# Performance work log

Hardware: AMD Instinct MI355X
Metric: run time of the kernel (lower is better)

The kernel has to match this reference:

```python
import jax, jax.numpy as jnp
import numpy as np

B, L, E, H = 32, 2048, 512, 512


def setup_inputs() -> dict:
    key = jax.random.key(0)
    k1, k2, k3, k4 = jax.random.split(key, 4)
    encodings = jax.random.normal(k1, (B, L, E), dtype=jnp.float32)
    lengths = jax.random.randint(k2, (B,), 1, L + 1, dtype=jnp.int32)
    # Glorot-ish scaled params
    W_h = jax.random.normal(k3, (E, H), dtype=jnp.float32) / np.sqrt(E)
    b_h = jnp.zeros((H,), dtype=jnp.float32)
    W_c = jax.random.normal(k4, (H, E), dtype=jnp.float32) / np.sqrt(H)
    return {"encodings": encodings, "lengths": lengths, "W_h": W_h, "b_h": b_h, "W_c": W_c}


def reference(encodings, lengths, W_h, b_h, W_c):
    # encodings: [B, L, E] padded ragged pack; lengths: [B] valid lengths
    mask = jnp.arange(encodings.shape[1])[None, :] < lengths[:, None]  # [B, L]
    # hidden_layer with tanh nonlinearity (TimeDistributedLinear)
    h = jnp.tanh(jnp.einsum('ble,eh->blh', encodings, W_h) + b_h)  # [B, L, H]
    # context_vector (no bias) -> per-feature attention logits [B, L, E]
    att = jnp.einsum('blh,he->ble', h, W_c)
    # timedistributed_softmax: softmax over time axis per sample, per feature
    att = jnp.where(mask[:, :, None], att, -jnp.inf)
    att = jax.nn.softmax(att, axis=1)  # padded positions get weight 0
    # weighted sum over time -> [B, E], then unsqueeze(1)
    out = jnp.sum(att * encodings, axis=1)[:, None, :]  # [B, 1, E]
    return out
```

## Files before the change

### kernel.cpp

```cpp
#include <hip/hip_runtime.h>
#include <math.h>

#define BB 32
#define LL 2048
#define EE 512
#define HH 512

typedef __bf16 bf16_t;
typedef bf16_t bf16x8 __attribute__((ext_vector_type(8)));
typedef float f32x4 __attribute__((ext_vector_type(4)));
typedef unsigned short u16x8 __attribute__((ext_vector_type(8)));

__device__ __forceinline__ unsigned short f2bf(float f) {
  unsigned int u = __builtin_bit_cast(unsigned int, f);
  unsigned int r = (u + 0x7FFFu + ((u >> 16) & 1u)) >> 16;
  return (unsigned short)r;
}
__device__ __forceinline__ float bf2f(unsigned short s) {
  unsigned int u = ((unsigned int)s) << 16;
  return __builtin_bit_cast(float, u);
}
__device__ __forceinline__ bf16x8 ld_frag(const unsigned short* p) {
  u16x8 raw = *(const u16x8*)p;
  return __builtin_bit_cast(bf16x8, raw);
}
__device__ __forceinline__ float tanh_fast(float x) {
  x = fminf(fmaxf(x, -15.f), 15.f);
  float e2 = __expf(2.f * x);
  return (e2 - 1.f) / (e2 + 1.f);
}

__device__ __forceinline__ void frag_issue(const unsigned short* __restrict__ g,
                                           int k0, bf16x8 f[4]) {
#pragma unroll
  for (int i = 0; i < 4; i++) f[i] = ld_frag(g + (size_t)i * 16 * 512 + k0);
}

#define G1_HALF(F, W, PF, PFB) do {                                             \
    if (PF) frag_issue(baseW, (((W) + 3 + phase) & 15) * 32, PFB);              \
    const int k0_ = (((W) + phase) & 15) * 32;                                  \
    const bf16x8 b0_ = ld_frag(&encA[(l15     ) * 520 + k0_ + quad * 8]);       \
    const bf16x8 b1_ = ld_frag(&encA[(16 + l15) * 520 + k0_ + quad * 8]);       \
    const bf16x8 b2_ = ld_frag(&encA[(32 + l15) * 520 + k0_ + quad * 8]);       \
    const bf16x8 b3_ = ld_frag(&encA[(48 + l15) * 520 + k0_ + quad * 8]);       \
    _Pragma("unroll")                                                           \
    for (int t_ = 0; t_ < 4; t_++) {                                            \
      acc[t_ * 4 + 0] = __builtin_amdgcn_mfma_f32_16x16x32_bf16(F[t_], b0_, acc[t_ * 4 + 0], 0, 0, 0); \
      acc[t_ * 4 + 1] = __builtin_amdgcn_mfma_f32_16x16x32_bf16(F[t_], b1_, acc[t_ * 4 + 1], 0, 0, 0); \
      acc[t_ * 4 + 2] = __builtin_amdgcn_mfma_f32_16x16x32_bf16(F[t_], b2_, acc[t_ * 4 + 2], 0, 0, 0); \
      acc[t_ * 4 + 3] = __builtin_amdgcn_mfma_f32_16x16x32_bf16(F[t_], b3_, acc[t_ * 4 + 3], 0, 0, 0); \
    }                                                                           \
  } while (0)

#define G2_HALF(F, W, PF, PFB) do {                                             \
    if (PF) frag_issue(baseW, (((W) + 3 + phase) & 15) * 32, PFB);              \
    const int k0_ = (((W) + phase) & 15) * 32;                                  \
    const bf16x8 a0_ = ld_frag(&hS[(l15     ) * 520 + k0_ + quad * 8]);         \
    const bf16x8 a1_ = ld_frag(&hS[(16 + l15) * 520 + k0_ + quad * 8]);         \
    const bf16x8 a2_ = ld_frag(&hS[(32 + l15) * 520 + k0_ + quad * 8]);         \
    const bf16x8 a3_ = ld_frag(&hS[(48 + l15) * 520 + k0_ + quad * 8]);         \
    _Pragma("unroll")                                                           \
    for (int e_ = 0; e_ < 4; e_++) {                                            \
      acc[0 * 4 + e_] = __builtin_amdgcn_mfma_f32_16x16x32_bf16(a0_, F[e_], acc[0 * 4 + e_], 0, 0, 0); \
      acc[1 * 4 + e_] = __builtin_amdgcn_mfma_f32_16x16x32_bf16(a1_, F[e_], acc[1 * 4 + e_], 0, 0, 0); \
      acc[2 * 4 + e_] = __builtin_amdgcn_mfma_f32_16x16x32_bf16(a2_, F[e_], acc[2 * 4 + e_], 0, 0, 0); \
      acc[3 * 4 + e_] = __builtin_amdgcn_mfma_f32_16x16x32_bf16(a3_, F[e_], acc[3 * 4 + e_], 0, 0, 0); \
    }                                                                           \
  } while (0)

__global__ __launch_bounds__(256) void prep_w(
    const float* __restrict__ Wh, const float* __restrict__ Wc,
    unsigned short* __restrict__ WhT, unsigned short* __restrict__ WcT,
    int* __restrict__ q)
{
  if (blockIdx.x == 0 && blockIdx.y == 0 && threadIdx.x == 0) *q = 0;
  const float* src = blockIdx.y ? Wc : Wh;
  unsigned short* dst = blockIdx.y ? WcT : WhT;
  const int tr = (blockIdx.x >> 3) * 64;
  const int tc = (blockIdx.x & 7) * 64;
  const int tid = threadIdx.x;
  __shared__ float tile[64][65];
  for (int i = tid; i < 64 * 16; i += 256) {
    const int r = i >> 4, c4 = (i & 15) << 2;
    const float4 v = *(const float4*)(src + (size_t)(tr + r) * 512 + tc + c4);
    tile[r][c4 + 0] = v.x; tile[r][c4 + 1] = v.y;
    tile[r][c4 + 2] = v.z; tile[r][c4 + 3] = v.w;
  }
  __syncthreads();
  for (int i = tid; i < 64 * 16; i += 256) {
    const int r = i >> 4, c4 = (i & 15) << 2;
    ushort4 pk;
    pk.x = f2bf(tile[c4 + 0][r]); pk.y = f2bf(tile[c4 + 1][r]);
    pk.z = f2bf(tile[c4 + 2][r]); pk.w = f2bf(tile[c4 + 3][r]);
    *(ushort4*)(dst + (size_t)(tc + r) * 512 + tr + c4) = pk;
  }
}

__global__ __launch_bounds__(512, 2) void attn_main(
    const float* __restrict__ enc, const int* __restrict__ lens,
    const unsigned short* __restrict__ WhT, const float* __restrict__ bh,
    const unsigned short* __restrict__ WcT,
    float* __restrict__ pm, float* __restrict__ ps, float* __restrict__ po,
    int* __restrict__ q, int C, int Lc)
{
  const int tid  = threadIdx.x;
  const int wave = tid >> 6;
  const int lane = tid & 63;
  const int quad = lane >> 4;
  const int l15  = lane & 15;
  const int wbase = wave * 64;

  __shared__ __align__(16) unsigned short encA[64 * 520];
  __shared__ __align__(16) unsigned short hS[64 * 520];
  __shared__ __align__(16) float bhS[512];
  __shared__ int itemS;

  bhS[tid] = bh[tid];
  const int nitems = 32 * C;

#pragma unroll 1
  for (;;) {
    __syncthreads();
    if (tid == 0) itemS = atomicAdd(q, 1);
    __syncthreads();
    const int item = itemS;
    if (item >= nitems) break;
    const int b = item & 31;
    const int c = item >> 5;
    const int n = lens[b];
    const int l0 = c * Lc;
    const int nvalid = min(n - l0, Lc);
    if (nvalid <= 0) continue;

    const int phase = (item + wave) & 15;

    float stM[4], stS[4], stO[4];
#pragma unroll
    for (int et = 0; et < 4; et++) { stM[et] = -1e30f; stS[et] = 0.f; stO[et] = 0.f; }

    f32x4 acc[16];

#pragma unroll 1
    for (int r0 = 0; r0 < nvalid; r0 += 64) {
      const float* encRow = enc + ((size_t)b * LL + l0 + r0) * EE;
      for (int i = tid; i < 64 * 128; i += 512) {
        const int m = i >> 7, e4 = (i & 127) << 2;
        const float4 v = *(const float4*)(encRow + (size_t)m * EE + e4);
        ushort4 pk;
        pk.x = f2bf(v.x); pk.y = f2bf(v.y); pk.z = f2bf(v.z); pk.w = f2bf(v.w);
        *(ushort4*)&encA[m * 520 + e4] = pk;
      }
      __syncthreads();

#pragma unroll
      for (int i = 0; i < 16; i++) acc[i] = (f32x4){0.f, 0.f, 0.f, 0.f};
      {
        const unsigned short* baseW = WhT + (size_t)(wbase + l15) * 512 + quad * 8;
        bf16x8 f0[4], f1[4], f2[4], f3[4];
        frag_issue(baseW, ((0 + phase) & 15) * 32, f0);
        frag_issue(baseW, ((1 + phase) & 15) * 32, f1);
        frag_issue(baseW, ((2 + phase) & 15) * 32, f2);
#pragma unroll 1
        for (int i = 0; i < 4; i++) {
          const int w = i * 4;
          const bool pf = (i < 3);
          G1_HALF(f0, w + 0, true, f3);
          G1_HALF(f1, w + 1, pf,   f0);
          G1_HALF(f2, w + 2, pf,   f1);
          G1_HALF(f3, w + 3, pf,   f2);
        }
      }

#pragma unroll
      for (int t = 0; t < 4; t++) {
        const f32x4 bv = *(const f32x4*)&bhS[wbase + t * 16 + quad * 4];
#pragma unroll
        for (int mt = 0; mt < 4; mt++) {
          ushort4 pk;
          pk.x = f2bf(tanh_fast(acc[t * 4 + mt][0] + bv[0]));
          pk.y = f2bf(tanh_fast(acc[t * 4 + mt][1] + bv[1]));
          pk.z = f2bf(tanh_fast(acc[t * 4 + mt][2] + bv[2]));
          pk.w = f2bf(tanh_fast(acc[t * 4 + mt][3] + bv[3]));
          *(ushort4*)&hS[(mt * 16 + l15) * 520 + wbase + t * 16 + quad * 4] = pk;
        }
      }
      __syncthreads();

#pragma unroll
      for (int i = 0; i < 16; i++) acc[i] = (f32x4){0.f, 0.f, 0.f, 0.f};
      {
        const unsigned short* baseW = WcT + (size_t)(wbase + l15) * 512 + quad * 8;
        bf16x8 f0[4], f1[4], f2[4], f3[4];
        frag_issue(baseW, ((0 + phase) & 15) * 32, f0);
        frag_issue(baseW, ((1 + phase) & 15) * 32, f1);
        frag_issue(baseW, ((2 + phase) & 15) * 32, f2);
#pragma unroll 1
        for (int i = 0; i < 4; i++) {
          const int w = i * 4;
          const bool pf = (i < 3);
          G2_HALF(f0, w + 0, true, f3);
          G2_HALF(f1, w + 1, pf,   f0);
          G2_HALF(f2, w + 2, pf,   f1);
          G2_HALF(f3, w + 3, pf,   f2);
        }
      }

#pragma unroll
      for (int et = 0; et < 4; et++) {
        const int e = wbase + et * 16 + l15;
        float lm = -1e30f;
#pragma unroll
        for (int mt = 0; mt < 4; mt++)
#pragma unroll
          for (int r = 0; r < 4; r++) {
            const float vv = (r0 + mt * 16 + quad * 4 + r) < nvalid ? acc[mt * 4 + et][r] : -1e30f;
            lm = fmaxf(lm, vv);
          }
        lm = fmaxf(lm, __shfl_xor(lm, 16));
        lm = fmaxf(lm, __shfl_xor(lm, 32));
        float ls = 0.f, lo = 0.f;
#pragma unroll
        for (int mt = 0; mt < 4; mt++)
#pragma unroll
          for (int r = 0; r < 4; r++) {
            const float vv = (r0 + mt * 16 + quad * 4 + r) < nvalid ? acc[mt * 4 + et][r] : -1e30f;
            const float p  = __expf(vv - lm);
            const float ev = bf2f(encA[(mt * 16 + quad * 4 + r) * 520 + e]);
            ls += p;
            lo += p * ev;
          }
        ls += __shfl_xor(ls, 16); ls += __shfl_xor(ls, 32);
        lo += __shfl_xor(lo, 16); lo += __shfl_xor(lo, 32);
        const float Mn = fmaxf(stM[et], lm);
        const float sc = __expf(stM[et] - Mn);
        const float st = __expf(lm - Mn);
        stS[et] = stS[et] * sc + ls * st;
        stO[et] = stO[et] * sc + lo * st;
        stM[et] = Mn;
      }
      __syncthreads();
    }

    if (quad == 0) {
      const size_t base = ((size_t)b * C + c) * EE;
#pragma unroll
      for (int et = 0; et < 4; et++) {
        const int e = wbase + et * 16 + l15;
        pm[base + e] = stM[et];
        ps[base + e] = stS[et];
        po[base + e] = stO[et];
      }
    }
  }
}

__global__ __launch_bounds__(256) void attn_combine(
    const float* __restrict__ pm, const float* __restrict__ ps,
    const float* __restrict__ po, const int* __restrict__ lens,
    float* __restrict__ out, int C, int Lc)
{
  const int b  = blockIdx.y;
  const int e  = blockIdx.x * 64 + (threadIdx.x & 63);
  const int g  = threadIdx.x >> 6;
  const int n  = lens[b];
  const int cmax = min(C, (n + Lc - 1) / Lc);

  float M = -1e30f, S = 0.f, O = 0.f;
  for (int c = g; c < cmax; c += 4) {
    const size_t base = ((size_t)b * C + c) * EE;
    const float m = pm[base + e];
    const float s = ps[base + e];
    const float o = po[base + e];
    const float Mn  = fmaxf(M, m);
    const float sc0 = __expf(M - Mn);
    const float sc1 = __expf(m - Mn);
    S = S * sc0 + s * sc1;
    O = O * sc0 + o * sc1;
    M = Mn;
  }

  __shared__ float sM[4][64], sS[4][64], sO[4][64];
  sM[g][threadIdx.x & 63] = M;
  sS[g][threadIdx.x & 63] = S;
  sO[g][threadIdx.x & 63] = O;
  __syncthreads();

  if (g == 0) {
    const int le = threadIdx.x & 63;
    float Mt = sM[0][le], St = sS[0][le], Ot = sO[0][le];
#pragma unroll
    for (int gg = 1; gg < 4; gg++) {
      const float m = sM[gg][le];
      const float Mn  = fmaxf(Mt, m);
      const float sc0 = __expf(Mt - Mn);
      const float sc1 = __expf(m - Mn);
      St = St * sc0 + sS[gg][le] * sc1;
      Ot = Ot * sc0 + sO[gg][le] * sc1;
      Mt = Mn;
    }
    out[(size_t)b * EE + e] = Ot / St;
  }
}

extern "C" void kernel_launch(void* const* d_in, const int* in_sizes, int n_in,
                              void* d_out, int out_size, void* d_ws, size_t ws_size,
                              hipStream_t stream) {
  const float* enc  = (const float*)d_in[0];
  const int*   lens = (const int*)d_in[1];
  const float* Wh   = (const float*)d_in[2];
  const float* bh   = (const float*)d_in[3];
  const float* Wc   = (const float*)d_in[4];
  float* out = (float*)d_out;

  const size_t wbytes = (size_t)512 * 512 * sizeof(unsigned short);
  int C = 32;
  while (C > 8 && ws_size < (size_t)3 * BB * C * EE * sizeof(float) + 2 * wbytes + 64)
    C >>= 1;
  const int Lc = LL / C;

  float* pm = (float*)d_ws;
  float* ps = pm + (size_t)BB * C * EE;
  float* po = ps + (size_t)BB * C * EE;
  unsigned short* WhT = (unsigned short*)(po + (size_t)BB * C * EE);
  unsigned short* WcT = WhT + (size_t)512 * 512;
  int* q = (int*)(WcT + (size_t)512 * 512);

  prep_w<<<dim3(64, 2), 256, 0, stream>>>(Wh, Wc, WhT, WcT, q);
  attn_main<<<dim3(256), 512, 0, stream>>>(enc, lens, WhT, bh, WcT, pm, ps, po, q, C, Lc);
  attn_combine<<<dim3(8, BB), 256, 0, stream>>>(pm, ps, po, lens, out, C, Lc);
}
```

Before: 313.5 us.

## Split attention block across 16 waves with half-width column tiles

```diff
diff --git a/kernel.cpp b/kernel.cpp
--- a/kernel.cpp
+++ b/kernel.cpp
@@ -30,42 +30,43 @@
   return (e2 - 1.f) / (e2 + 1.f);
 }
 
-__device__ __forceinline__ void frag_issue(const unsigned short* __restrict__ g,
-                                           int k0, bf16x8 f[4]) {
-#pragma unroll
-  for (int i = 0; i < 4; i++) f[i] = ld_frag(g + (size_t)i * 16 * 512 + k0);
-}
-
-#define G1_HALF(F, W, PF, PFB) do {                                             \
-    if (PF) frag_issue(baseW, (((W) + 3 + phase) & 15) * 32, PFB);              \
+__device__ __forceinline__ void frag_issue2(const unsigned short* __restrict__ g,
+                                            int k0, bf16x8 f[2]) {
+#pragma unroll
+  for (int i = 0; i < 2; i++) f[i] = ld_frag(g + (size_t)i * 16 * 512 + k0);
+}
+
+#define G1_HALF(F, W, PF) do {                                                  \
     const int k0_ = (((W) + phase) & 15) * 32;                                  \
     const bf16x8 b0_ = ld_frag(&encA[(l15     ) * 520 + k0_ + quad * 8]);       \
     const bf16x8 b1_ = ld_frag(&encA[(16 + l15) * 520 + k0_ + quad * 8]);       \
     const bf16x8 b2_ = ld_frag(&encA[(32 + l15) * 520 + k0_ + quad * 8]);       \
     const bf16x8 b3_ = ld_frag(&encA[(48 + l15) * 520 + k0_ + quad * 8]);       \
     _Pragma("unroll")                                                           \
-    for (int t_ = 0; t_ < 4; t_++) {                                            \
+    for (int t_ = 0; t_ < 2; t_++) {                                            \
       acc[t_ * 4 + 0] = __builtin_amdgcn_mfma_f32_16x16x32_bf16(F[t_], b0_, acc[t_ * 4 + 0], 0, 0, 0); \
       acc[t_ * 4 + 1] = __builtin_amdgcn_mfma_f32_16x16x32_bf16(F[t_], b1_, acc[t_ * 4 + 1], 0, 0, 0); \
       acc[t_ * 4 + 2] = __builtin_amdgcn_mfma_f32_16x16x32_bf16(F[t_], b2_, acc[t_ * 4 + 2], 0, 0, 0); \
       acc[t_ * 4 + 3] = __builtin_amdgcn_mfma_f32_16x16x32_bf16(F[t_], b3_, acc[t_ * 4 + 3], 0, 0, 0); \
     }                                                                           \
+    if (PF) frag_issue2(baseW, (((W) + 2 + phase) & 15) * 32, F);               \
   } while (0)
 
-#define G2_HALF(F, W, PF, PFB) do {                                             \
-    if (PF) frag_issue(baseW, (((W) + 3 + phase) & 15) * 32, PFB);              \
+#define G2_HALF(F, W, PF) do {                                                  \
     const int k0_ = (((W) + phase) & 15) * 32;                                  \
     const bf16x8 a0_ = ld_frag(&hS[(l15     ) * 520 + k0_ + quad * 8]);         \
     const bf16x8 a1_ = ld_frag(&hS[(16 + l15) * 520 + k0_ + quad * 8]);         \
     const bf16x8 a2_ = ld_frag(&hS[(32 + l15) * 520 + k0_ + quad * 8]);         \
     const bf16x8 a3_ = ld_frag(&hS[(48 + l15) * 520 + k0_ + quad * 8]);         \
     _Pragma("unroll")                                                           \
-    for (int e_ = 0; e_ < 4; e_++) {                                            \
-      acc[0 * 4 + e_] = __builtin_amdgcn_mfma_f32_16x16x32_bf16(a0_, F[e_], acc[0 * 4 + e_], 0, 0, 0); \
-      acc[1 * 4 + e_] = __builtin_amdgcn_mfma_f32_16x16x32_bf16(a1_, F[e_], acc[1 * 4 + e_], 0, 0, 0); \
-      acc[2 * 4 + e_] = __builtin_amdgcn_mfma_f32_16x16x32_bf16(a2_, F[e_], acc[2 * 4 + e_], 0, 0, 0); \
-      acc[3 * 4 + e_] = __builtin_amdgcn_mfma_f32_16x16x32_bf16(a3_, F[e_], acc[3 * 4 + e_], 0, 0, 0); \
+    for (int e_ = 0; e_ < 2; e_++) {                                            \
+      acc[0 * 2 + e_] = __builtin_amdgcn_mfma_f32_16x16x32_bf16(a0_, F[e_], acc[0 * 2 + e_], 0, 0, 0); \
+      acc[2 + 2 * 1 * e_ + 0] = acc[2 + 2 * 1 * e_ + 0];                        \
+      acc[1 * 2 + e_] = __builtin_amdgcn_mfma_f32_16x16x32_bf16(a1_, F[e_], acc[1 * 2 + e_], 0, 0, 0); \
+      acc[2 * 2 + e_] = __builtin_amdgcn_mfma_f32_16x16x32_bf16(a2_, F[e_], acc[2 * 2 + e_], 0, 0, 0); \
+      acc[3 * 2 + e_] = __builtin_amdgcn_mfma_f32_16x16x32_bf16(a3_, F[e_], acc[3 * 2 + e_], 0, 0, 0); \
     }                                                                           \
+    if (PF) frag_issue2(baseW, (((W) + 2 + phase) & 15) * 32, F);               \
   } while (0)
 
 __global__ __launch_bounds__(256) void prep_w(
@@ -96,7 +97,7 @@
   }
 }
 
-__global__ __launch_bounds__(512, 2) void attn_main(
+__global__ __launch_bounds__(1024, 4) void attn_main(
     const float* __restrict__ enc, const int* __restrict__ lens,
     const unsigned short* __restrict__ WhT, const float* __restrict__ bh,
     const unsigned short* __restrict__ WcT,
@@ -104,18 +105,18 @@
     int* __restrict__ q, int C, int Lc)
 {
   const int tid  = threadIdx.x;
+  const int lane = tid & 63;
   const int wave = tid >> 6;
-  const int lane = tid & 63;
   const int quad = lane >> 4;
   const int l15  = lane & 15;
-  const int wbase = wave * 64;
+  const int wbase = wave * 32;
 
   __shared__ __align__(16) unsigned short encA[64 * 520];
   __shared__ __align__(16) unsigned short hS[64 * 520];
   __shared__ __align__(16) float bhS[512];
   __shared__ int itemS;
 
-  bhS[tid] = bh[tid];
+  if (tid < 512) bhS[tid] = bh[tid];
   const int nitems = 32 * C;
 
 #pragma unroll 1
@@ -134,16 +135,16 @@
 
     const int phase = (item + wave) & 15;
 
-    float stM[4], stS[4], stO[4];
-#pragma unroll
-    for (int et = 0; et < 4; et++) { stM[et] = -1e30f; stS[et] = 0.f; stO[et] = 0.f; }
-
-    f32x4 acc[16];
+    float stM[2], stS[2], stO[2];
+#pragma unroll
+    for (int et = 0; et < 2; et++) { stM[et] = -1e30f; stS[et] = 0.f; stO[et] = 0.f; }
+
+    f32x4 acc[8];
 
 #pragma unroll 1
     for (int r0 = 0; r0 < nvalid; r0 += 64) {
       const float* encRow = enc + ((size_t)b * LL + l0 + r0) * EE;
-      for (int i = tid; i < 64 * 128; i += 512) {
+      for (int i = tid; i < 64 * 128; i += 1024) {
         const int m = i >> 7, e4 = (i & 127) << 2;
         const float4 v = *(const float4*)(encRow + (size_t)m * EE + e4);
         ushort4 pk;
@@ -153,26 +154,21 @@
       __syncthreads();
 
 #pragma unroll
-      for (int i = 0; i < 16; i++) acc[i] = (f32x4){0.f, 0.f, 0.f, 0.f};
+      for (int i = 0; i < 8; i++) acc[i] = (f32x4){0.f, 0.f, 0.f, 0.f};
       {
         const unsigned short* baseW = WhT + (size_t)(wbase + l15) * 512 + quad * 8;
-        bf16x8 f0[4], f1[4], f2[4], f3[4];
-        frag_issue(baseW, ((0 + phase) & 15) * 32, f0);
-        frag_issue(baseW, ((1 + phase) & 15) * 32, f1);
-        frag_issue(baseW, ((2 + phase) & 15) * 32, f2);
+        bf16x8 fA[2], fB[2];
+        frag_issue2(baseW, ((0 + phase) & 15) * 32, fA);
+        frag_issue2(baseW, ((1 + phase) & 15) * 32, fB);
 #pragma unroll 1
-        for (int i = 0; i < 4; i++) {
-          const int w = i * 4;
-          const bool pf = (i < 3);
-          G1_HALF(f0, w + 0, true, f3);
-          G1_HALF(f1, w + 1, pf,   f0);
-          G1_HALF(f2, w + 2, pf,   f1);
-          G1_HALF(f3, w + 3, pf,   f2);
+        for (int kk = 0; kk < 16; kk += 2) {
+          G1_HALF(fA, kk + 0, (kk + 2 < 16));
+          G1_HALF(fB, kk + 1, (kk + 3 < 16));
         }
       }
 
 #pragma unroll
-      for (int t = 0; t < 4; t++) {
+      for (int t = 0; t < 2; t++) {
         const f32x4 bv = *(const f32x4*)&bhS[wbase + t * 16 + quad * 4];
 #pragma unroll
         for (int mt = 0; mt < 4; mt++) {
@@ -187,33 +183,28 @@
       __syncthreads();
 
 #pragma unroll
-      for (int i = 0; i < 16; i++) acc[i] = (f32x4){0.f, 0.f, 0.f, 0.f};
+      for (int i = 0; i < 8; i++) acc[i] = (f32x4){0.f, 0.f, 0.f, 0.f};
       {
         const unsigned short* baseW = WcT + (size_t)(wbase + l15) * 512 + quad * 8;
-        bf16x8 f0[4], f1[4], f2[4], f3[4];
-        frag_issue(baseW, ((0 + phase) & 15) * 32, f0);
-        frag_issue(baseW, ((1 + phase) & 15) * 32, f1);
-        frag_issue(baseW, ((2 + phase) & 15) * 32, f2);
+        bf16x8 fA[2], fB[2];
+        frag_issue2(baseW, ((0 + phase) & 15) * 32, fA);
+        frag_issue2(baseW, ((1 + phase) & 15) * 32, fB);
 #pragma unroll 1
-        for (int i = 0; i < 4; i++) {
-          const int w = i * 4;
-          const bool pf = (i < 3);
-          G2_HALF(f0, w + 0, true, f3);
-          G2_HALF(f1, w + 1, pf,   f0);
-          G2_HALF(f2, w + 2, pf,   f1);
-          G2_HALF(f3, w + 3, pf,   f2);
+        for (int kk = 0; kk < 16; kk += 2) {
+          G2_HALF(fA, kk + 0, (kk + 2 < 16));
+          G2_HALF(fB, kk + 1, (kk + 3 < 16));
         }
       }
 
 #pragma unroll
-      for (int et = 0; et < 4; et++) {
+      for (int et = 0; et < 2; et++) {
         const int e = wbase + et * 16 + l15;
         float lm = -1e30f;
 #pragma unroll
         for (int mt = 0; mt < 4; mt++)
 #pragma unroll
           for (int r = 0; r < 4; r++) {
-            const float vv = (r0 + mt * 16 + quad * 4 + r) < nvalid ? acc[mt * 4 + et][r] : -1e30f;
+            const float vv = (r0 + mt * 16 + quad * 4 + r) < nvalid ? acc[mt * 2 + et][r] : -1e30f;
             lm = fmaxf(lm, vv);
           }
         lm = fmaxf(lm, __shfl_xor(lm, 16));
@@ -223,7 +214,7 @@
         for (int mt = 0; mt < 4; mt++)
 #pragma unroll
           for (int r = 0; r < 4; r++) {
-            const float vv = (r0 + mt * 16 + quad * 4 + r) < nvalid ? acc[mt * 4 + et][r] : -1e30f;
+            const float vv = (r0 + mt * 16 + quad * 4 + r) < nvalid ? acc[mt * 2 + et][r] : -1e30f;
             const float p  = __expf(vv - lm);
             const float ev = bf2f(encA[(mt * 16 + quad * 4 + r) * 520 + e]);
             ls += p;
@@ -244,7 +235,7 @@
     if (quad == 0) {
       const size_t base = ((size_t)b * C + c) * EE;
 #pragma unroll
-      for (int et = 0; et < 4; et++) {
+      for (int et = 0; et < 2; et++) {
         const int e = wbase + et * 16 + l15;
         pm[base + e] = stM[et];
         ps[base + e] = stS[et];
@@ -326,6 +317,6 @@
   int* q = (int*)(WcT + (size_t)512 * 512);
 
   prep_w<<<dim3(64, 2), 256, 0, stream>>>(Wh, Wc, WhT, WcT, q);
-  attn_main<<<dim3(256), 512, 0, stream>>>(enc, lens, WhT, bh, WcT, pm, ps, po, q, C, Lc);
+  attn_main<<<dim3(256), 1024, 0, stream>>>(enc, lens, WhT, bh, WcT, pm, ps, po, q, C, Lc);
   attn_combine<<<dim3(8, BB), 256, 0, stream>>>(pm, ps, po, lens, out, C, Lc);
 }
```

Measured after the change: 308.5 us. Within noise of the previous version (-1.6%).
